# Performance work log

Measured on AMD Instinct MI355X. Metric: run time of the kernel, lower is better.

The kernel has to match this reference:

```python
import jax, jax.numpy as jnp
import numpy as np

B, F_IN, GRID, D, C = 32768, 64, 8, 16, 10
N = GRID * GRID          # 64 nodes
HID = N * D              # 1024
ATOMS = 2
LN_EPS = 1e-5
EPS = 1e-8


def _layernorm(h):
    mu = h.mean(-1, keepdims=True)
    var = h.var(-1, keepdims=True)
    return (h - mu) / jnp.sqrt(var + LN_EPS)


def _regulator(sig, w1, b1, g, be, w2, b2):
    # Linear -> LayerNorm -> Tanh -> Linear -> Sigmoid
    h = jnp.tanh(_layernorm(sig @ w1.T + b1) * g + be)
    return jax.nn.sigmoid(h @ w2.T + b2)


def _reg_params(key, in_dim):
    k = jax.random.split(key, 4)
    return (jax.random.normal(k[0], (16, in_dim)) * 0.3,
            jax.random.normal(k[1], (16,)) * 0.1,
            jnp.ones((16,)), jnp.zeros((16,)),
            jax.random.normal(k[2], (3, 16)) * 0.3,
            jax.random.normal(k[3], (3,)) * 0.1)


def setup_inputs() -> dict:
    key = jax.random.key(0)
    ks = jax.random.split(key, 16)
    # 2D grid 4-neighbour adjacency mask (constant)
    mask = np.zeros((N, N), np.float32)
    for i in range(N):
        r, c = divmod(i, GRID)
        if r > 0: mask[i, i - GRID] = 1
        if r < GRID - 1: mask[i, i + GRID] = 1
        if c > 0: mask[i, i - 1] = 1
        if c < GRID - 1: mask[i, i + 1] = 1
    pr = _reg_params(ks[10], 3)
    cr = _reg_params(ks[11], 3)
    sr = _reg_params(ks[12], 3)
    scr = _reg_params(ks[13], 2)
    inp = {
        "x": jax.random.normal(ks[0], (B, F_IN)),
        "W_embed": jax.random.normal(ks[1], (HID, F_IN)) * 0.1,
        "b_embed": jnp.zeros((HID,)),
        "adj_weights": jax.random.normal(ks[2], (N, N)) * 0.1,
        "adj_mask": jnp.asarray(mask),
        "V_slow": jax.random.normal(ks[3], (D, D)) * 0.1,
        "W_slow": jax.random.normal(ks[4], (D, D)) * 0.1,
        "gate_w": jax.random.normal(ks[5], (1, D)) * 0.3,
        "gate_b": jnp.zeros((1,)),
        "W_fast": jax.random.normal(ks[6], (D, D)) * 0.05,  # buffer, eval mode (no Hebbian update)
        "basis": jax.random.normal(ks[7], (ATOMS, D)) * 0.5,
        "Wq": jax.random.normal(ks[8], (D, D)) * 0.2,
        "sc_w1": jax.random.normal(ks[9], (8, HID)) * 0.05,
        "sc_w2": jax.random.normal(ks[14], (4, 8)) * 0.3,
        "W_read": jax.random.normal(ks[15], (C, HID)) * 0.05,
        "b_read": jnp.zeros((C,)),
    }
    for pre, p in (("pr", pr), ("cr", cr), ("sr", sr), ("scr", scr)):
        for nm, v in zip(("w1", "b1", "g", "be", "w2", "b2"), p):
            inp[pre + "_" + nm] = v
    return inp


def reference(x, W_embed, b_embed, adj_weights, adj_mask,
              pr_w1, pr_b1, pr_g, pr_be, pr_w2, pr_b2,
              V_slow, W_slow, gate_w, gate_b, W_fast,
              cr_w1, cr_b1, cr_g, cr_be, cr_w2, cr_b2,
              basis, Wq,
              sr_w1, sr_b1, sr_g, sr_be, sr_w2, sr_b2,
              sc_w1, sc_w2,
              scr_w1, scr_b1, scr_g, scr_be, scr_w2, scr_b2,
              W_read, b_read):
    Bx = x.shape[0]
    x_embed = (x @ W_embed.T + b_embed).reshape(Bx, N, D)

    # --- AutoregulatedPlasticity adjacency ---
    sig = jnp.stack([jnp.var(x, ddof=1), jnp.abs(x_embed).mean(),
                     jnp.linalg.norm(adj_weights)])[None]
    pl = _regulator(sig, pr_w1, pr_b1, pr_g, pr_be, pr_w2, pr_b2)[0]
    adj = jax.nn.sigmoid(adj_weights * pl[0]) * adj_mask
    adj = adj / jnp.clip(adj.sum(1, keepdims=True), 1e-6, None)
    x_agg = jnp.einsum('nm,bmd->bnd', adj, x_embed)

    # --- AutoregulatedContinuum (eval: W_fast fixed) ---
    xf = x_agg.reshape(-1, D)           # [B*N, D]
    v = xf @ V_slow.T
    sig = jnp.stack([jnp.var(xf, ddof=1), jnp.abs(v).mean(),
                     jnp.linalg.norm(W_slow)])[None]
    ctrl = _regulator(sig, cr_w1, cr_b1, cr_g, cr_be, cr_w2, cr_b2)[0]
    gate = jax.nn.sigmoid(v @ gate_w.T + gate_b) * ctrl[0]   # [B*N, 1]
    fast_out = xf @ W_fast.T
    x_proc = (gate * (v + fast_out * ctrl[2])).reshape(Bx, N, D)

    # --- AutoregulatedSymbiotic, applied per node (vmapped over node axis) ---
    ortho = jnp.linalg.norm(basis @ basis.T - jnp.eye(ATOMS))
    scale = D ** 0.5 + EPS

    def sym_one(xn):  # xn: [B, D]
        w = jax.nn.softmax((xn @ Wq.T) @ basis.T / scale, axis=-1)  # [B, ATOMS]
        ent = -(w * jnp.log(w + EPS)).sum(-1).mean()
        sig_n = jnp.stack([jnp.var(xn, ddof=1), ent, ortho])[None]
        infl = _regulator(sig_n, sr_w1, sr_b1, sr_g, sr_be, sr_w2, sr_b2)[0, 0]
        return (1.0 - infl) * xn + infl * (w @ basis), ent

    refined, ents = jax.vmap(sym_one)(x_proc.transpose(1, 0, 2))  # [N,B,D]
    x_proc = refined.transpose(1, 0, 2)
    entropy = ents[-1]  # torch loop keeps the last node's entropy

    x_flat = x_proc.reshape(Bx, HID)
    logits = x_flat @ W_read.T + b_read

    # --- AutoregulatedSupConHead (entropy.item() -> detached scalar) ---
    sigc = jnp.stack([jnp.var(x_flat, ddof=1),
                      jax.lax.stop_gradient(entropy)])[None]
    gain = _regulator(sigc, scr_w1, scr_b1, scr_g, scr_be, scr_w2, scr_b2)[0, 0]
    proj = (jax.nn.relu(x_flat @ sc_w1.T) @ sc_w2.T) * gain
    return logits, proj, entropy, ortho
```

## Files before the change

kernel.cpp:

```cpp
#include <hip/hip_runtime.h>

typedef unsigned short u16;
typedef unsigned long long u64;
typedef __attribute__((ext_vector_type(8))) short short8;
typedef __attribute__((ext_vector_type(4))) float f32x4;

#define MFMA16(a,b,c) __builtin_amdgcn_mfma_f32_16x16x32_bf16(a,b,c,0,0,0)

#define B_SZ   32768
#define NNODE  64
#define NB_PAIR (B_SZ*NNODE)
#define OUT_PROJ   327680
#define OUT_ENT    458752
#define OUT_ORTHO  458753

#define OFF_SCAL   ((size_t)0)
#define OFF_ADJ    ((size_t)512)
#define OFF_BEFF   (OFF_ADJ  + 8192u)
#define OFF_WEFF   (OFF_BEFF + 4096u)
#define OFF_WCAT   (OFF_WEFF + 131072u)
#define OFF_S1     (OFF_WCAT + 65536u)
#define OFF_S2     (OFF_S1   + 12288u)
#define OFF_S3     (OFF_S2   + 12288u)
#define OFF_S4     (OFF_S3   + 2048u*192u*4u)
#define OFF_H      (OFF_S4   + 8192u)
#define OFF_W01    (OFF_H    + (size_t)B_SZ*8u*4u)
#define OFF_CAN    (OFF_W01  + (size_t)NB_PAIR*4u)

#define CAN_X      0u
#define CAN_WEMB   2097152u
#define CAN_WREAD  (CAN_WEMB + 65536u)
#define CAN_SCW1   (CAN_WREAD + 10240u)
#define CAN_SMALL  (CAN_SCW1 + 8192u)
#define CAN_TOTAL  (CAN_SMALL + 11008u)
#define OFF_BEX    (((OFF_CAN + (size_t)CAN_TOTAL*2u) + 63u) & ~(size_t)63u)
#define OFF_WET    (OFF_BEX + 48u*16u*2u)
#define OFF_VW     (OFF_WET + 131072u)
#define OFF_VB     (OFF_VW  + 131072u)
#define OFF_WC     (OFF_VB  + 4096u)
#define OFF_SW     (OFF_WC  + 131072u)
#define OFF_BC2    (OFF_SW  + 24576u)
#define OFF_SB     (OFF_BC2 + 4096u)
#define OFF_DR     (OFF_SB  + 1024u)
#define WS_NEEDED  (OFF_DR  + 192u*8u)

__device__ __forceinline__ float bf2f(u16 u){
    unsigned v = ((unsigned)u) << 16;
    return __builtin_bit_cast(float, v);
}
__device__ __forceinline__ u16 f2bf(float f){
    unsigned u = __builtin_bit_cast(unsigned, f);
    u += 0x7FFFu + ((u >> 16) & 1u);
    return (u16)(u >> 16);
}
__device__ __forceinline__ float sigm(float x){ return 1.f/(1.f + expf(-x)); }
__device__ __forceinline__ u16 conv_one(const void* src, int i, int isfp32){
    return isfp32 ? f2bf(((const float*)src)[i]) : ((const u16*)src)[i];
}
__device__ __forceinline__ void store_out(void* dout, int idx, float v, int isfp32){
    if (isfp32) ((float*)dout)[idx] = v;
    else        ((u16*)dout)[idx]   = f2bf(v);
}
__device__ __forceinline__ double blk_red(double v, double* sred, int tid){
    #pragma unroll
    for (int off = 32; off > 0; off >>= 1) v += __shfl_xor(v, off);
    if ((tid & 63) == 0) sred[tid >> 6] = v;
    __syncthreads();
    double r = sred[0] + sred[1] + sred[2] + sred[3];
    __syncthreads();
    return r;
}
__device__ __forceinline__ void blk_red4(double* v, double* sred, int tid){
    #pragma unroll
    for (int off = 32; off > 0; off >>= 1){
        v[0] += __shfl_xor(v[0], off);
        v[1] += __shfl_xor(v[1], off);
        v[2] += __shfl_xor(v[2], off);
        v[3] += __shfl_xor(v[3], off);
    }
    if ((tid & 63) == 0){
        int w = tid >> 6;
        sred[w*4+0] = v[0]; sred[w*4+1] = v[1];
        sred[w*4+2] = v[2]; sred[w*4+3] = v[3];
    }
    __syncthreads();
    #pragma unroll
    for (int k = 0; k < 4; ++k)
        v[k] = sred[0*4+k] + sred[1*4+k] + sred[2*4+k] + sred[3*4+k];
    __syncthreads();
}

__device__ void run_regulator(const u16* w1, const u16* b1, const u16* g,
                              const u16* be, const u16* w2, const u16* b2,
                              const float* sig, int in_dim, float* out)
{
    float h[16];
    float mu = 0.f;
    for (int i = 0; i < 16; ++i){
        float a = bf2f(b1[i]);
        for (int j = 0; j < in_dim; ++j) a += sig[j]*bf2f(w1[i*in_dim + j]);
        h[i] = a; mu += a;
    }
    mu *= 0.0625f;
    float var = 0.f;
    for (int i = 0; i < 16; ++i){ float d = h[i]-mu; var += d*d; }
    var *= 0.0625f;
    float inv = 1.f / sqrtf(var + 1e-5f);
    for (int i = 0; i < 16; ++i){
        float hn = (h[i]-mu)*inv;
        h[i] = tanhf(hn*bf2f(g[i]) + bf2f(be[i]));
    }
    for (int c = 0; c < 3; ++c){
        float o = bf2f(b2[c]);
        for (int i = 0; i < 16; ++i) o += h[i]*bf2f(w2[c*16 + i]);
        out[c] = sigm(o);
    }
}

__device__ __forceinline__ int probe_isfp32(const u16* xraw, int tid, int* sred)
{
    int c = 0;
    #pragma unroll
    for (int j = 0; j < 4; ++j){
        u16 u = xraw[(tid*4 + j)*2];
        int e = (u >> 7) & 0xFF;
        if (u == 0 || (e >= 90 && e <= 140)) c++;
    }
    #pragma unroll
    for (int off = 32; off > 0; off >>= 1) c += __shfl_xor(c, off);
    if ((tid & 63) == 0) sred[tid >> 6] = c;
    __syncthreads();
    int tot = sred[0]+sred[1]+sred[2]+sred[3];
    __syncthreads();
    return tot < 614;
}

struct SmallTab { const void* src[36]; int cnt[36]; int off[36]; };
__global__ __launch_bounds__(256) void kc_all(SmallTab t,
    const void* x, const void* wemb, const void* wread_raw, const void* scw1_raw,
    const void* vslow_raw, const void* gatew_raw,
    u16* can, float* scal, u16* wcat, u16* wembT, u16* bex)
{
    __shared__ int sred[4];
    int b = blockIdx.x, tid = threadIdx.x;
    int isfp32 = probe_isfp32((const u16*)x, tid, sred);
    if (b == 0 && tid == 0) scal[127] = isfp32 ? 1.0f : 0.0f;
    if (b < 1024){
        int gid = b*256 + tid, stride = 1024*256;
        for (int i = gid; i < 2097152; i += stride) can[CAN_X + i]     = conv_one(x, i, isfp32);
        for (int i = gid; i < 65536;   i += stride) can[CAN_WEMB + i]  = conv_one(wemb, i, isfp32);
        for (int i = gid; i < 10240;   i += stride) can[CAN_WREAD + i] = conv_one(wread_raw, i, isfp32);
        for (int i = gid; i < 8192;    i += stride) can[CAN_SCW1 + i]  = conv_one(scw1_raw, i, isfp32);
    } else if (b < 1040){
        int gid = (b-1024)*256 + tid, stride = 16*256;
        for (int e = 0; e < 36; ++e){
            const void* s = t.src[e];
            u16* d = can + t.off[e];
            int n = t.cnt[e];
            for (int i = gid; i < n; i += stride) d[i] = conv_one(s, i, isfp32);
        }
    } else if (b < 1168){
        int idx = (b-1040)*256 + tid;
        int row = idx >> 10, k = idx & 1023;
        u16 v = 0;
        if (row < 10)      v = conv_one(wread_raw, row*1024 + k, isfp32);
        else if (row < 18) v = conv_one(scw1_raw, (row-10)*1024 + k, isfp32);
        int lo = k & 31;
        int khw = ((lo >> 2) & 3)*8 + ((lo >> 4) << 2) + (lo & 3);
        wcat[row*1024 + (k & ~31) + khw] = v;
    } else if (b < 1424){
        int idx = (b-1168)*256 + tid;
        int m = idx >> 10, jj = idx & 1023;
        wembT[jj*64 + m] = conv_one(wemb, m*1024 + jj, isfp32);
    } else {
        if (tid < 16){
            float a = 0.f;
            for (int i = 0; i < 16; ++i)
                a += bf2f(conv_one(gatew_raw, i, isfp32))*bf2f(conv_one(vslow_raw, i*16+tid, isfp32));
            bex[32*16+tid] = f2bf(a);
        }
    }
}

__global__ __launch_bounds__(256) void k1_embed(const u16* x, const u16* wemb,
                                                const u16* bemb, float* s1)
{
    __shared__ float red[12];
    int tid = threadIdx.x, wave = tid>>6, lane = tid&63;
    int m = lane&15, quad = lane>>4;
    int cg = blockIdx.x & 15, rc = blockIdx.x >> 4;
    short8 b0[4], b1[4];
    float bias[4];
    #pragma unroll
    for (int s = 0; s < 4; ++s){
        int col = cg*64 + s*16 + m;
        b0[s] = *(const short8*)(wemb + col*64 + quad*8);
        b1[s] = *(const short8*)(wemb + col*64 + quad*8 + 32);
        bias[s] = bf2f(bemb[col]);
    }
    float sx = 0.f, sxx = 0.f, sabs = 0.f;
    const u16* xbase = x + (size_t)(rc*512 + wave*128 + m)*64 + quad*8;
    #pragma unroll 4
    for (int it = 0; it < 8; ++it){
        const u16* xr = xbase + (size_t)it*16*64;
        short8 a0 = *(const short8*)xr;
        short8 a1 = *(const short8*)(xr + 32);
        if (cg == 0){
            #pragma unroll
            for (int j = 0; j < 8; ++j){
                float f0 = bf2f((u16)a0[j]); sx += f0; sxx += f0*f0;
                float f1 = bf2f((u16)a1[j]); sx += f1; sxx += f1*f1;
            }
        }
        #pragma unroll
        for (int s = 0; s < 4; ++s){
            f32x4 zc = {0.f,0.f,0.f,0.f};
            f32x4 c = MFMA16(a0, b0[s], zc);
            c = MFMA16(a1, b1[s], c);
            #pragma unroll
            for (int r = 0; r < 4; ++r)
                sabs += fabsf(c[r]+bias[s]);
        }
    }
    #pragma unroll
    for (int off = 32; off > 0; off >>= 1){
        sx   += __shfl_xor(sx, off);
        sxx  += __shfl_xor(sxx, off);
        sabs += __shfl_xor(sabs, off);
    }
    if (lane == 0){ red[wave*3] = sx; red[wave*3+1] = sxx; red[wave*3+2] = sabs; }
    __syncthreads();
    if (tid == 0){
        for (int k = 0; k < 3; ++k)
            s1[blockIdx.x*3 + k] = red[k] + red[3+k] + red[6+k] + red[9+k];
    }
}

__global__ __launch_bounds__(256) void k2_adj(const u16* adjw, const u16* adjm, const u16* bemb,
    const u16* w1, const u16* b1, const u16* g, const u16* be, const u16* w2, const u16* b2,
    const float* s1, float* scal, u16* adjb, float* beff)
{
    __shared__ double sred[16];
    __shared__ float raw[4096];
    __shared__ float rowsum[64];
    __shared__ float bembs[1024];
    __shared__ float pl0s;
    int tid = threadIdx.x;
    for (int i = tid; i < 1024; i += 256) bembs[i] = bf2f(bemb[i]);
    double v[4] = {0,0,0,0};
    for (int i = tid; i < 1024; i += 256){
        v[0] += (double)s1[i*3]; v[1] += (double)s1[i*3+1]; v[2] += (double)s1[i*3+2];
    }
    for (int i = tid; i < 4096; i += 256){ float f = bf2f(adjw[i]); v[3] += (double)(f*f); }
    blk_red4(v, sred, tid);
    if (tid == 0){
        double nx = 2097152.0;
        float sg[3];
        sg[0] = (float)((v[1] - v[0]*v[0]/nx)/(nx - 1.0));
        sg[1] = (float)(v[2] / 33554432.0);
        sg[2] = sqrtf((float)v[3]);
        float o[3];
        run_regulator(w1,b1,g,be,w2,b2, sg, 3, o);
        scal[0] = o[0]; pl0s = o[0];
    }
    __syncthreads();
    float pl0 = pl0s;
    for (int i = tid; i < 4096; i += 256)
        raw[i] = sigm(bf2f(adjw[i])*pl0) * bf2f(adjm[i]);
    __syncthreads();
    if (tid < 64){
        float r = 0.f;
        for (int mc = 0; mc < 64; ++mc) r += raw[tid*64 + mc];
        rowsum[tid] = fmaxf(r, 1e-6f);
    }
    __syncthreads();
    for (int i = tid; i < 4096; i += 256) adjb[i] = f2bf(raw[i] / rowsum[i>>6]);
    for (int o = tid; o < 1024; o += 256){
        int n = o >> 4, d = o & 15;
        float a = 0.f;
        for (int m = 0; m < 64; ++m) a += raw[n*64+m]*bembs[m*16+d];
        beff[o] = a / rowsum[n];
    }
}

__global__ __launch_bounds__(256) void k2b_mfma(const u16* adjb, const u16* wembT, u16* weff)
{
    int tid = threadIdx.x, wave = tid>>6, lane = tid&63;
    int m = lane&15, quad = lane>>4;
    const u16* ar = adjb + (wave*16 + m)*64 + quad*8;
    short8 a0 = *(const short8*)ar;
    short8 a1 = *(const short8*)(ar + 32);
    int col = blockIdx.x*16 + m;
    const u16* br = wembT + col*64 + quad*8;
    short8 b0 = *(const short8*)br;
    short8 b1 = *(const short8*)(br + 32);
    f32x4 acc = {0.f,0.f,0.f,0.f};
    acc = MFMA16(a0, b0, acc);
    acc = MFMA16(a1, b1, acc);
    #pragma unroll
    for (int r = 0; r < 4; ++r)
        weff[(size_t)(wave*16 + quad*4 + r)*1024 + blockIdx.x*16 + m] = f2bf(acc[r]);
}

__global__ __launch_bounds__(256) void kvw(const u16* vslow, const u16* weff, const float* beff,
                                           u16* vw, float* vbias)
{
    __shared__ float Vs[256];
    int tid = threadIdx.x, b = blockIdx.x;
    Vs[tid] = bf2f(vslow[tid]);
    __syncthreads();
    if (b < 256){
        int idx = b*256 + tid;
        int j = idx >> 6, kf = idx & 63;
        int n = j >> 4, i = j & 15;
        float a = 0.f;
        #pragma unroll
        for (int d = 0; d < 16; ++d) a += Vs[i*16+d]*bf2f(weff[(size_t)(n*16+d)*64 + kf]);
        vw[(size_t)j*64 + kf] = f2bf(a);
    } else {
        int o = (b-256)*256 + tid;
        int n = o >> 4, i = o & 15;
        float a = 0.f;
        #pragma unroll
        for (int d = 0; d < 16; ++d) a += Vs[i*16+d]*beff[n*16+d];
        vbias[o] = a;
    }
}

__global__ __launch_bounds__(256) void k3_stats(const u16* x, const u16* weff, const float* beff,
                                                const u16* vw, const float* vbias, float* s2)
{
    __shared__ float red[12];
    int tid = threadIdx.x, wave = tid>>6, lane = tid&63;
    int m = lane&15, quad = lane>>4;
    int cg = blockIdx.x & 15, rc = blockIdx.x >> 4;
    short8 wb0[4], wb1[4], vb0[4], vb1[4];
    float bev[4], vbv[4];
    #pragma unroll
    for (int s = 0; s < 4; ++s){
        int col = cg*64 + s*16 + m;
        wb0[s] = *(const short8*)(weff + (size_t)col*64 + quad*8);
        wb1[s] = *(const short8*)(weff + (size_t)col*64 + quad*8 + 32);
        vb0[s] = *(const short8*)(vw + (size_t)col*64 + quad*8);
        vb1[s] = *(const short8*)(vw + (size_t)col*64 + quad*8 + 32);
        bev[s] = beff[col];
        vbv[s] = vbias[col];
    }
    float psum=0.f, pssq=0.f, pabsv=0.f;
    const u16* xbase = x + (size_t)(rc*512 + wave*128 + m)*64 + quad*8;
    #pragma unroll 4
    for (int it = 0; it < 8; ++it){
        const u16* xr = xbase + (size_t)it*16*64;
        short8 a0 = *(const short8*)xr;
        short8 a1 = *(const short8*)(xr + 32);
        #pragma unroll
        for (int s = 0; s < 4; ++s){
            f32x4 zc = {0.f,0.f,0.f,0.f};
            f32x4 c = MFMA16(a0, wb0[s], zc);
            c = MFMA16(a1, wb1[s], c);
            f32x4 w = MFMA16(a0, vb0[s], zc);
            w = MFMA16(a1, vb1[s], w);
            #pragma unroll
            for (int r = 0; r < 4; ++r){
                float f0 = c[r] + bev[s];
                psum += f0; pssq += f0*f0;
                pabsv += fabsf(w[r] + vbv[s]);
            }
        }
    }
    #pragma unroll
    for (int off = 32; off > 0; off >>= 1){
        psum  += __shfl_xor(psum, off);
        pssq  += __shfl_xor(pssq, off);
        pabsv += __shfl_xor(pabsv, off);
    }
    if (lane == 0){ red[wave*3] = psum; red[wave*3+1] = pssq; red[wave*3+2] = pabsv; }
    __syncthreads();
    if (tid == 0){
        for (int k = 0; k < 3; ++k)
            s2[blockIdx.x*3 + k] = red[k] + red[3+k] + red[6+k] + red[9+k];
    }
}

__global__ __launch_bounds__(256) void k3b_ctrl(const u16* wslow,
    const u16* vslow, const u16* wfast, const u16* wq, const u16* basis,
    const u16* w1, const u16* b1, const u16* g, const u16* be, const u16* w2, const u16* b2,
    const float* s2, float* scal, u16* bex)
{
    __shared__ double sred[16];
    __shared__ float ctrl2s;
    int tid = threadIdx.x;
    double v[4] = {0,0,0,0};
    for (int i = tid; i < 1024; i += 256){
        v[0] += (double)s2[i*3]; v[1] += (double)s2[i*3+1]; v[2] += (double)s2[i*3+2];
    }
    float wf = bf2f(wslow[tid]);
    v[3] = (double)(wf*wf);
    blk_red4(v, sred, tid);
    if (tid == 0){
        double M = 33554432.0;
        float sg[3];
        sg[0] = (float)((v[1] - v[0]*v[0]/M)/(M - 1.0));
        sg[1] = (float)(v[2] / M);
        sg[2] = sqrtf((float)v[3]);
        float o[3];
        run_regulator(w1,b1,g,be,w2,b2, sg, 3, o);
        scal[1] = o[0]; scal[2] = o[2];
        ctrl2s = o[2];
    }
    __syncthreads();
    float ctrl2 = ctrl2s;
    if (tid < 64){
        #pragma unroll
        for (int j = 0; j < 4; ++j){
            int idx = tid*4 + j;
            int d = idx >> 4, k = idx & 15;
            bex[(16+d)*16+k] = f2bf(bf2f(vslow[idx]) + ctrl2*bf2f(wfast[idx]));
        }
    } else if (tid < 96){
        int a = (tid-64) >> 4, k = (tid-64) & 15;
        float e = 0.f;
        for (int d = 0; d < 16; ++d){
            float bq = 0.f;
            for (int j = 0; j < 16; ++j) bq += bf2f(basis[a*16+j])*bf2f(wq[j*16+d]);
            e += bq*(bf2f(vslow[d*16+k]) + ctrl2*bf2f(wfast[d*16+k]));
        }
        bex[(33+a)*16+k] = f2bf(0.25f*e);
    }
}

__global__ __launch_bounds__(256) void kbw(const u16* bex, const u16* weff, const float* beff,
                                           const u16* gateb, u16* wc, u16* sw,
                                           float* bc, float* sb)
{
    __shared__ float BcL[256], gvL[16], e0L[16], e1L[16];
    int tid = threadIdx.x;
    if (tid < 256) BcL[tid] = bf2f(bex[(16 + (tid>>4))*16 + (tid&15)]);
    if (tid < 16){
        gvL[tid] = bf2f(bex[32*16+tid]);
        e0L[tid] = bf2f(bex[33*16+tid]);
        e1L[tid] = bf2f(bex[34*16+tid]);
    }
    __syncthreads();
    int id = blockIdx.x*256 + tid;
    if (id < 65536){
        int col = id >> 6, k = id & 63;
        int n = col >> 4, d = col & 15;
        float a = 0.f;
        #pragma unroll
        for (int dd = 0; dd < 16; ++dd)
            a += BcL[d*16+dd]*bf2f(weff[(size_t)(n*16+dd)*64 + k]);
        wc[(size_t)col*64 + k] = f2bf(a);
    } else if (id < 77824){
        int j2 = id - 65536;
        int scol = j2 >> 6, k = j2 & 63;
        int n = scol/3, j = scol - n*3;
        const float* sr = (j==0) ? gvL : (j==1) ? e0L : e1L;
        float a = 0.f;
        #pragma unroll
        for (int dd = 0; dd < 16; ++dd)
            a += sr[dd]*bf2f(weff[(size_t)(n*16+dd)*64 + k]);
        sw[(size_t)scol*64 + k] = f2bf(a);
    } else if (id < 78848){
        int col = id - 77824;
        int n = col >> 4, d = col & 15;
        float a = 0.f;
        #pragma unroll
        for (int dd = 0; dd < 16; ++dd) a += BcL[d*16+dd]*beff[n*16+dd];
        bc[col] = a;
    } else if (id < 79040){
        int s = id - 78848;
        int n = s/3, j = s - n*3;
        const float* sr = (j==0) ? gvL : (j==1) ? e0L : e1L;
        float a = 0.f;
        #pragma unroll
        for (int dd = 0; dd < 16; ++dd) a += sr[dd]*beff[n*16+dd];
        if (j == 0) a += bf2f(gateb[0]);
        sb[s] = a;
    }
}

#define SCP 193
#define GTP 65
__global__ __launch_bounds__(256) void k4_stats(const u16* x, const u16* wc, const u16* sw,
    const float* bc, const float* sb, const float* scal, unsigned* wpack, float* s3)
{
    __shared__ float sc[32*SCP];
    __shared__ float gt[32*GTP];
    __shared__ float entp[256];
    __shared__ float snode[128];
    int tid = threadIdx.x, wave = tid>>6, lane = tid&63;
    int m = lane&15, quad = lane>>4;
    int row0 = blockIdx.x*32;
    const u16* xrA = x + (size_t)(row0 + m)*64 + quad*8;
    short8 a0A = *(const short8*)xrA;
    short8 a1A = *(const short8*)(xrA + 32);
    const u16* xrB = xrA + 16*64;
    short8 a0B = *(const short8*)xrB;
    short8 a1B = *(const short8*)(xrB + 32);
    float ctrl0 = scal[1];
    #pragma unroll
    for (int tt = 0; tt < 3; ++tt){
        int ct = wave*3 + tt;
        int scol = ct*16 + m;
        const u16* br = sw + (size_t)scol*64 + quad*8;
        short8 b0 = *(const short8*)br;
        short8 b1 = *(const short8*)(br + 32);
        f32x4 zc = {0.f,0.f,0.f,0.f};
        f32x4 cA = MFMA16(a0A, b0, zc);
        cA = MFMA16(a1A, b1, cA);
        f32x4 cB = MFMA16(a0B, b0, zc);
        cB = MFMA16(a1B, b1, cB);
        float sbv = sb[scol];
        #pragma unroll
        for (int r = 0; r < 4; ++r){
            sc[(quad*4+r)*SCP + scol]      = cA[r] + sbv;
            sc[(16+quad*4+r)*SCP + scol]   = cB[r] + sbv;
        }
    }
    __syncthreads();
    {
        int n = tid & 63, rgrp = tid >> 6;
        float ent = 0.f;
        #pragma unroll
        for (int rr = 0; rr < 8; ++rr){
            int row = rgrp*8 + rr;
            float gd  = sc[row*SCP + 3*n];
            float e0d = sc[row*SCP + 3*n + 1];
            float e1d = sc[row*SCP + 3*n + 2];
            float gate = ctrl0 / (1.f + __expf(-gd));
            float l0 = gate*e0d, l1 = gate*e1d;
            float w1v = 1.f/(1.f + __expf(l0 - l1));
            float w0v = 1.f - w1v;
            ent += -(w0v*__logf(w0v + 1e-8f) + w1v*__logf(w1v + 1e-8f));
            gt[row*GTP + n] = gate;
            wpack[(size_t)(row0 + row)*64 + n] =
                ((unsigned)f2bf(w0v) << 16) | (unsigned)f2bf(gate);
        }
        entp[tid] = ent;
    }
    __syncthreads();
    #pragma unroll
    for (int tt = 0; tt < 16; ++tt){
        int n = wave*16 + tt;
        int col = n*16 + m;
        const u16* br = wc + (size_t)col*64 + quad*8;
        short8 b0 = *(const short8*)br;
        short8 b1 = *(const short8*)(br + 32);
        f32x4 zc = {0.f,0.f,0.f,0.f};
        f32x4 cA = MFMA16(a0A, b0, zc);
        cA = MFMA16(a1A, b1, cA);
        f32x4 cB = MFMA16(a0B, b0, zc);
        cB = MFMA16(a1B, b1, cB);
        float bcv = bc[col];
        float ps = 0.f, pq = 0.f;
        #pragma unroll
        for (int r = 0; r < 4; ++r){
            float gA  = gt[(quad*4+r)*GTP + n];
            float xpA = gA*(cA[r] + bcv);
            float gB  = gt[(16+quad*4+r)*GTP + n];
            float xpB = gB*(cB[r] + bcv);
            ps += xpA + xpB; pq += xpA*xpA + xpB*xpB;
        }
        #pragma unroll
        for (int off = 32; off > 0; off >>= 1){
            ps += __shfl_xor(ps, off);
            pq += __shfl_xor(pq, off);
        }
        if (lane == 0){ snode[n] = ps; snode[64+n] = pq; }
    }
    __syncthreads();
    if (tid < 192){
        float v;
        if (tid < 128) v = snode[tid];
        else { int n = tid-128; v = entp[n]+entp[64+n]+entp[128+n]+entp[192+n]; }
        s3[(size_t)blockIdx.x*192 + tid] = v;
    }
}

__global__ __launch_bounds__(256) void k5ab(const float* s3, const u16* basis,
    const u16* w1, const u16* b1, const u16* g, const u16* be, const u16* w2, const u16* b2,
    float* scal, void* dout)
{
    __shared__ double sred[12];
    int tid = threadIdx.x, n = blockIdx.x;
    int wave = tid >> 6, lane = tid & 63;
    double a0 = 0, a1 = 0, a2 = 0;
    for (int i = tid; i < 1024; i += 256){
        const float* r = s3 + (size_t)i*192;
        a0 += (double)r[n]; a1 += (double)r[64+n]; a2 += (double)r[128+n];
    }
    #pragma unroll
    for (int off = 32; off > 0; off >>= 1){
        a0 += __shfl_xor(a0, off);
        a1 += __shfl_xor(a1, off);
        a2 += __shfl_xor(a2, off);
    }
    if (lane == 0){ sred[wave*3] = a0; sred[wave*3+1] = a1; sred[wave*3+2] = a2; }
    __syncthreads();
    if (tid == 0){
        int isfp32 = scal[127] != 0.f;
        double sum = sred[0]+sred[3]+sred[6]+sred[9];
        double ssq = sred[1]+sred[4]+sred[7]+sred[10];
        double ent = sred[2]+sred[5]+sred[8]+sred[11];
        double Mn = 524288.0;
        float varn = (float)((ssq - sum*sum/Mn)/(Mn - 1.0));
        float entm = (float)(ent / 32768.0);
        float b0[16], b1v[16];
        for (int d = 0; d < 16; ++d){ b0[d] = bf2f(basis[d]); b1v[d] = bf2f(basis[16+d]); }
        float g00=0.f, g01=0.f, g11=0.f;
        for (int d = 0; d < 16; ++d){
            g00 += b0[d]*b0[d]; g01 += b0[d]*b1v[d]; g11 += b1v[d]*b1v[d];
        }
        float ortho = sqrtf((g00-1.f)*(g00-1.f) + 2.f*g01*g01 + (g11-1.f)*(g11-1.f));
        float sg[3] = {varn, entm, ortho};
        float o[3];
        run_regulator(w1,b1,g,be,w2,b2, sg, 3, o);
        scal[4+n] = o[0];
        if (n == 63){ scal[68] = entm;  store_out(dout, OUT_ENT,   entm,  isfp32); }
        if (n == 0) { scal[69] = ortho; store_out(dout, OUT_ORTHO, ortho, isfp32); }
    }
}

__global__ __launch_bounds__(128, 2) void k6_read(const u16* x, const unsigned* wpack,
    const u16* wc, const float* bc, const u16* wcatP,
    const u16* basis, const u16* bread, const float* scal,
    void* dout, float* hbuf, float* s4)
{
    __shared__ unsigned gwP[64*65];
    __shared__ float bc_s[1024];
    __shared__ float infl_s[64], b0s[16], b1s[16], brd[16];
    __shared__ float red[4];
    int tid = threadIdx.x;
    int isfp32 = scal[127] != 0.f;
    for (int i = tid; i < 4096; i += 128)
        gwP[(i >> 6)*65 + (i & 63)] = wpack[(size_t)blockIdx.x*4096 + i];
    for (int i = tid; i < 1024; i += 128) bc_s[i] = bc[i];
    if (tid < 64) infl_s[tid] = scal[4+tid];
    if (tid < 16){
        b0s[tid] = bf2f(basis[tid]);
        b1s[tid] = bf2f(basis[16+tid]);
        brd[tid] = (tid < 10) ? bf2f(bread[tid]) : 0.f;
    }
    __syncthreads();
    int wave = tid>>6, lane = tid&63;
    int m = lane&15, quad = lane>>4;
    int rowA = blockIdx.x*64 + wave*32 + m;
    const u16* xrA = x + (size_t)rowA*64 + quad*8;
    short8 a0A = *(const short8*)xrA;
    short8 a1A = *(const short8*)(xrA + 32);
    const u16* xrB = xrA + 16*64;
    short8 a0B = *(const short8*)xrB;
    short8 a1B = *(const short8*)(xrB + 32);
    float b0d[4], b1d[4];
    #pragma unroll
    for (int r = 0; r < 4; ++r){ b0d[r] = b0s[quad*4+r]; b1d[r] = b1s[quad*4+r]; }
    const unsigned* gwA = gwP + (wave*32 + m)*65;
    const unsigned* gwB = gwA + 16*65;
    f32x4 acc0A = {0.f,0.f,0.f,0.f}, acc1A = {0.f,0.f,0.f,0.f};
    f32x4 acc0B = {0.f,0.f,0.f,0.f}, acc1B = {0.f,0.f,0.f,0.f};
    float psum = 0.f, pssq = 0.f;
    for (int c8 = 0; c8 < 8; ++c8){
        unsigned pdaA[8], pdbA[8], pdaB[8], pdbB[8];
        #pragma unroll
        for (int hf = 0; hf < 2; ++hf){
            short8 wf0[4], wf1[4];
            f32x4 bc4[4];
            unsigned gvA[4], gvB[4];
            float fiv[4];
            #pragma unroll
            for (int j = 0; j < 4; ++j){
                int n = c8*8 + hf*4 + j;
                int col = n*16 + m;
                const u16* br = wc + (size_t)col*64 + quad*8;
                wf0[j] = *(const short8*)br;
                wf1[j] = *(const short8*)(br + 32);
                bc4[j] = *(const f32x4*)(bc_s + n*16 + quad*4);
                gvA[j] = gwA[n];
                gvB[j] = gwB[n];
                fiv[j] = infl_s[n];
            }
            f32x4 cA[4], cB[4];
            #pragma unroll
            for (int j = 0; j < 4; ++j){
                f32x4 zc = {0.f,0.f,0.f,0.f};
                cA[j] = MFMA16(wf0[j], a0A, zc);
                cB[j] = MFMA16(wf0[j], a0B, zc);
            }
            #pragma unroll
            for (int j = 0; j < 4; ++j){
                cA[j] = MFMA16(wf1[j], a1A, cA[j]);
                cB[j] = MFMA16(wf1[j], a1B, cB[j]);
            }
            #pragma unroll
            for (int j = 0; j < 4; ++j){
                int t = hf*4 + j;
                float fi = fiv[j];
                {
                    float gate = bf2f((u16)(gvA[j] & 0xFFFFu));
                    float w0v  = bf2f((u16)(gvA[j] >> 16));
                    float Am   = (1.f - fi)*gate;
                    float fw0 = fi*w0v;
                    float fw1 = fi - fw0;
                    float xf[4];
                    #pragma unroll
                    for (int r = 0; r < 4; ++r){
                        float base = fw0*b0d[r] + fw1*b1d[r];
                        float v = Am*(cA[j][r] + bc4[j][r]) + base;
                        psum += v; pssq += v*v;
                        xf[r] = v;
                    }
                    pdaA[t] = (unsigned)f2bf(xf[0]) | ((unsigned)f2bf(xf[1]) << 16);
                    pdbA[t] = (unsigned)f2bf(xf[2]) | ((unsigned)f2bf(xf[3]) << 16);
                }
                {
                    float gate = bf2f((u16)(gvB[j] & 0xFFFFu));
                    float w0v  = bf2f((u16)(gvB[j] >> 16));
                    float Am   = (1.f - fi)*gate;
                    float fw0 = fi*w0v;
                    float fw1 = fi - fw0;
                    float xf[4];
                    #pragma unroll
                    for (int r = 0; r < 4; ++r){
                        float base = fw0*b0d[r] + fw1*b1d[r];
                        float v = Am*(cB[j][r] + bc4[j][r]) + base;
                        psum += v; pssq += v*v;
                        xf[r] = v;
                    }
                    pdaB[t] = (unsigned)f2bf(xf[0]) | ((unsigned)f2bf(xf[1]) << 16);
                    pdbB[t] = (unsigned)f2bf(xf[2]) | ((unsigned)f2bf(xf[3]) << 16);
                }
            }
        }
        #pragma unroll
        for (int kk = 0; kk < 4; ++kk){
            int4 awA = make_int4((int)pdaA[2*kk], (int)pdbA[2*kk],
                                 (int)pdaA[2*kk+1], (int)pdbA[2*kk+1]);
            int4 awB = make_int4((int)pdaB[2*kk], (int)pdbB[2*kk],
                                 (int)pdaB[2*kk+1], (int)pdbB[2*kk+1]);
            short8 afA = __builtin_bit_cast(short8, awA);
            short8 afB = __builtin_bit_cast(short8, awB);
            const u16* wb = wcatP + m*1024 + c8*128 + kk*32 + quad*8;
            short8 bb0 = *(const short8*)wb;
            short8 bb1 = *(const short8*)(wb + 16*1024);
            acc0A = MFMA16(afA, bb0, acc0A);
            acc0B = MFMA16(afB, bb0, acc0B);
            acc1A = MFMA16(afA, bb1, acc1A);
            acc1B = MFMA16(afB, bb1, acc1B);
        }
    }
    int rowbaseA = blockIdx.x*64 + wave*32 + quad*4;
    #pragma unroll
    for (int r = 0; r < 4; ++r){
        int rowgA = rowbaseA + r;
        if (m < 10) store_out(dout, rowgA*10 + m, acc0A[r] + brd[m], isfp32);
        else        hbuf[rowgA*8 + (m-10)] = fmaxf(acc0A[r], 0.f);
        if (m < 2)  hbuf[rowgA*8 + 6 + m]  = fmaxf(acc1A[r], 0.f);
        int rowgB = rowgA + 16;
        if (m < 10) store_out(dout, rowgB*10 + m, acc0B[r] + brd[m], isfp32);
        else        hbuf[rowgB*8 + (m-10)] = fmaxf(acc0B[r], 0.f);
        if (m < 2)  hbuf[rowgB*8 + 6 + m]  = fmaxf(acc1B[r], 0.f);
    }
    #pragma unroll
    for (int off = 32; off > 0; off >>= 1){
        psum += __shfl_xor(psum, off);
        pssq += __shfl_xor(pssq, off);
    }
    if (lane == 0){ red[wave] = psum; red[2+wave] = pssq; }
    __syncthreads();
    if (tid == 0){
        s4[blockIdx.x*2]   = red[0]+red[1];
        s4[blockIdx.x*2+1] = red[2]+red[3];
    }
}

__global__ __launch_bounds__(256) void k8_proj(const float* hbuf, const u16* scw2,
    const u16* w1, const u16* b1, const u16* g, const u16* be, const u16* w2, const u16* b2,
    const float* s4, const float* scal, void* dout)
{
    __shared__ double sred[4];
    __shared__ float w2s[32];
    __shared__ float gains;
    int tid = threadIdx.x;
    int isfp32 = scal[127] != 0.f;
    if (tid < 32) w2s[tid] = bf2f(scw2[tid]);
    double s=0, ss=0;
    for (int i = tid; i < 512; i += 256){ s += (double)s4[i*2]; ss += (double)s4[i*2+1]; }
    double S  = blk_red(s,  sred, tid);
    double SS = blk_red(ss, sred, tid);
    if (tid == 0){
        double M = 33554432.0;
        float sg[2];
        sg[0] = (float)((SS - S*S/M)/(M - 1.0));
        sg[1] = scal[68];
        float o[3];
        run_regulator(w1,b1,g,be,w2,b2, sg, 2, o);
        gains = o[0];
    }
    __syncthreads();
    float gain = gains;
    int b = blockIdx.x*256 + tid;
    const float* h = hbuf + (size_t)b*8;
    float hv[8];
    #pragma unroll
    for (int k = 0; k < 8; ++k) hv[k] = h[k];
    #pragma unroll
    for (int i = 0; i < 4; ++i){
        float o = 0.f;
        #pragma unroll
        for (int k = 0; k < 8; ++k) o += hv[k]*w2s[i*8+k];
        store_out(dout, OUT_PROJ + b*4 + i, o*gain, isfp32);
    }
}

extern "C" void kernel_launch(void* const* d_in, const int* in_sizes, int n_in,
                              void* d_out, int out_size, void* d_ws, size_t ws_size,
                              hipStream_t stream)
{
    if (ws_size < WS_NEEDED) return;

    char* ws = (char*)d_ws;
    float* scal  = (float*)(ws + OFF_SCAL);
    u16*   adjb  = (u16*)  (ws + OFF_ADJ);
    float* beff  = (float*)(ws + OFF_BEFF);
    u16*   weff  = (u16*)  (ws + OFF_WEFF);
    u16*   wcat  = (u16*)  (ws + OFF_WCAT);
    float* s1    = (float*)(ws + OFF_S1);
    float* s2    = (float*)(ws + OFF_S2);
    float* s3    = (float*)(ws + OFF_S3);
    float* s4    = (float*)(ws + OFF_S4);
    float* hbuf  = (float*)(ws + OFF_H);
    unsigned* wpack = (unsigned*)(ws + OFF_W01);
    u16*   can   = (u16*)  (ws + OFF_CAN);
    u16*   bex   = (u16*)  (ws + OFF_BEX);
    u16*   wembT = (u16*)  (ws + OFF_WET);
    u16*   vw    = (u16*)  (ws + OFF_VW);
    float* vbias = (float*)(ws + OFF_VB);
    u16*   wc    = (u16*)  (ws + OFF_WC);
    u16*   sw    = (u16*)  (ws + OFF_SW);
    float* bc    = (float*)(ws + OFF_BC2);
    float* sb    = (float*)(ws + OFF_SB);

    static const int sidx[36] = {2,3,4,5,6,7,8,9,10,11,13,15,
        16,17,18,19,20,21, 22,23,24,25,26,27, 28,29,30,31,32,33, 34,35,36,37,38,39};
    static const int scnt[36] = {1024,4096,4096,256,256,16,1,256,32,256,32,10,
        48,16,16,16,48,3, 48,16,16,16,48,3, 48,16,16,16,48,3, 32,16,16,16,48,3};
    SmallTab t;
    const u16* canp[40];
    {
        int off = (int)CAN_SMALL;
        for (int j = 0; j < 36; ++j){
            t.src[j] = d_in[sidx[j]];
            t.cnt[j] = scnt[j];
            t.off[j] = off;
            canp[sidx[j]] = can + off;
            off += (scnt[j] + 7) & ~7;
        }
    }
    canp[0]  = can + CAN_X;
    canp[1]  = can + CAN_WEMB;
    canp[12] = can + CAN_SCW1;
    canp[14] = can + CAN_WREAD;

    const u16* pr_[6]; const u16* cr_[6]; const u16* sr_[6]; const u16* sc_[6];
    for (int i = 0; i < 6; ++i){
        pr_[i] = canp[16+i]; cr_[i] = canp[22+i];
        sr_[i] = canp[28+i]; sc_[i] = canp[34+i];
    }

    kc_all  <<<1425,256, 0, stream>>>(t, d_in[0], d_in[1], d_in[14], d_in[12],
                 d_in[5], d_in[7], can, scal, wcat, wembT, bex);
    k1_embed<<<1024,256, 0, stream>>>(canp[0], canp[1], canp[2], s1);
    k2_adj  <<<1,   256, 0, stream>>>(canp[3], canp[4], canp[2],
                 pr_[0],pr_[1],pr_[2],pr_[3],pr_[4],pr_[5], s1, scal, adjb, beff);
    k2b_mfma<<<64,  256, 0, stream>>>(adjb, wembT, weff);
    kvw     <<<260, 256, 0, stream>>>(canp[5], weff, beff, vw, vbias);
    k3_stats<<<1024,256, 0, stream>>>(canp[0], weff, beff, vw, vbias, s2);
    k3b_ctrl<<<1,   256, 0, stream>>>(canp[6], canp[5], canp[9], canp[11], canp[10],
                 cr_[0],cr_[1],cr_[2],cr_[3],cr_[4],cr_[5], s2, scal, bex);
    kbw     <<<312, 256, 0, stream>>>(bex, weff, beff, canp[8], wc, sw, bc, sb);
    k4_stats<<<1024,256, 0, stream>>>(canp[0], wc, sw, bc, sb, scal, wpack, s3);
    k5ab    <<<64,  256, 0, stream>>>(s3, canp[10],
                 sr_[0],sr_[1],sr_[2],sr_[3],sr_[4],sr_[5], scal, d_out);
    k6_read <<<512, 128, 0, stream>>>(canp[0], wpack, wc, bc, wcat, canp[10], canp[15],
                 scal, d_out, hbuf, s4);
    k8_proj <<<128, 256, 0, stream>>>(hbuf, canp[13],
                 sc_[0],sc_[1],sc_[2],sc_[3],sc_[4],sc_[5], s4, scal, d_out);
}
```

Before: 305.4 us.

## Double rows per wave in readout kernel and vectorize input conversion copies

The readout kernel now handles 128 rows per block (64 per wave, four 16-row tiles) instead of 64, so each loaded weight fragment is reused across four MFMA tiles. The grid is halved to 256 blocks and the final reduction loop is adjusted to match. Separately, the input conversion copies x and the large weights in 8-element vectors instead of one element at a time. The risks are higher register pressure from the extra accumulators and a grid of 256 blocks, which may underfill the GPU.

```diff
diff --git a/kernel.cpp b/kernel.cpp
--- a/kernel.cpp
+++ b/kernel.cpp
@@ -135,6 +135,26 @@
     return tot < 614;
 }
 
+__device__ __forceinline__ void copy_big(const void* src, u16* dst, int nvec,
+                                         int gid, int stride, int isfp32)
+{
+    if (!isfp32){
+        const short8* s = (const short8*)src;
+        for (int i = gid; i < nvec; i += stride) *(short8*)(dst + i*8) = s[i];
+    } else {
+        const f32x4* s = (const f32x4*)src;
+        for (int i = gid; i < nvec; i += stride){
+            f32x4 v0 = s[i*2], v1 = s[i*2+1];
+            u64 lo = (u64)f2bf(v0[0]) | ((u64)f2bf(v0[1])<<16) |
+                     ((u64)f2bf(v0[2])<<32) | ((u64)f2bf(v0[3])<<48);
+            u64 hi = (u64)f2bf(v1[0]) | ((u64)f2bf(v1[1])<<16) |
+                     ((u64)f2bf(v1[2])<<32) | ((u64)f2bf(v1[3])<<48);
+            *(u64*)(dst + i*8)     = lo;
+            *(u64*)(dst + i*8 + 4) = hi;
+        }
+    }
+}
+
 struct SmallTab { const void* src[36]; int cnt[36]; int off[36]; };
 __global__ __launch_bounds__(256) void kc_all(SmallTab t,
     const void* x, const void* wemb, const void* wread_raw, const void* scw1_raw,
@@ -147,10 +167,10 @@
     if (b == 0 && tid == 0) scal[127] = isfp32 ? 1.0f : 0.0f;
     if (b < 1024){
         int gid = b*256 + tid, stride = 1024*256;
-        for (int i = gid; i < 2097152; i += stride) can[CAN_X + i]     = conv_one(x, i, isfp32);
-        for (int i = gid; i < 65536;   i += stride) can[CAN_WEMB + i]  = conv_one(wemb, i, isfp32);
-        for (int i = gid; i < 10240;   i += stride) can[CAN_WREAD + i] = conv_one(wread_raw, i, isfp32);
-        for (int i = gid; i < 8192;    i += stride) can[CAN_SCW1 + i]  = conv_one(scw1_raw, i, isfp32);
+        copy_big(x,         can + CAN_X,     262144, gid, stride, isfp32);
+        copy_big(wemb,      can + CAN_WEMB,  8192,   gid, stride, isfp32);
+        copy_big(wread_raw, can + CAN_WREAD, 1280,   gid, stride, isfp32);
+        copy_big(scw1_raw,  can + CAN_SCW1,  1024,   gid, stride, isfp32);
     } else if (b < 1040){
         int gid = (b-1024)*256 + tid, stride = 16*256;
         for (int e = 0; e < 36; ++e){
@@ -622,19 +642,40 @@
     }
 }
 
+__device__ __forceinline__ void k6_epi(unsigned gv, float fi, f32x4 c, f32x4 bcv,
+    const float* b0d, const float* b1d, float& psum, float& pssq,
+    unsigned& lo, unsigned& hi)
+{
+    float gate = bf2f((u16)(gv & 0xFFFFu));
+    float w0v  = bf2f((u16)(gv >> 16));
+    float Am = (1.f - fi)*gate;
+    float fw0 = fi*w0v;
+    float fw1 = fi - fw0;
+    float xf[4];
+    #pragma unroll
+    for (int r = 0; r < 4; ++r){
+        float base = fw0*b0d[r] + fw1*b1d[r];
+        float v = Am*(c[r] + bcv[r]) + base;
+        psum += v; pssq += v*v;
+        xf[r] = v;
+    }
+    lo = (unsigned)f2bf(xf[0]) | ((unsigned)f2bf(xf[1]) << 16);
+    hi = (unsigned)f2bf(xf[2]) | ((unsigned)f2bf(xf[3]) << 16);
+}
+
 __global__ __launch_bounds__(128, 2) void k6_read(const u16* x, const unsigned* wpack,
     const u16* wc, const float* bc, const u16* wcatP,
     const u16* basis, const u16* bread, const float* scal,
     void* dout, float* hbuf, float* s4)
 {
-    __shared__ unsigned gwP[64*65];
+    __shared__ unsigned gwP[128*65];
     __shared__ float bc_s[1024];
     __shared__ float infl_s[64], b0s[16], b1s[16], brd[16];
     __shared__ float red[4];
     int tid = threadIdx.x;
     int isfp32 = scal[127] != 0.f;
-    for (int i = tid; i < 4096; i += 128)
-        gwP[(i >> 6)*65 + (i & 63)] = wpack[(size_t)blockIdx.x*4096 + i];
+    for (int i = tid; i < 8192; i += 128)
+        gwP[(i >> 6)*65 + (i & 63)] = wpack[(size_t)blockIdx.x*8192 + i];
     for (int i = tid; i < 1024; i += 128) bc_s[i] = bc[i];
     if (tid < 64) infl_s[tid] = scal[4+tid];
     if (tid < 16){
@@ -645,28 +686,31 @@
     __syncthreads();
     int wave = tid>>6, lane = tid&63;
     int m = lane&15, quad = lane>>4;
-    int rowA = blockIdx.x*64 + wave*32 + m;
+    int rowA = blockIdx.x*128 + wave*64 + m;
     const u16* xrA = x + (size_t)rowA*64 + quad*8;
-    short8 a0A = *(const short8*)xrA;
-    short8 a1A = *(const short8*)(xrA + 32);
-    const u16* xrB = xrA + 16*64;
-    short8 a0B = *(const short8*)xrB;
-    short8 a1B = *(const short8*)(xrB + 32);
+    short8 a0A = *(const short8*)xrA,            a1A = *(const short8*)(xrA + 32);
+    short8 a0B = *(const short8*)(xrA + 16*64),  a1B = *(const short8*)(xrA + 16*64 + 32);
+    short8 a0C = *(const short8*)(xrA + 32*64),  a1C = *(const short8*)(xrA + 32*64 + 32);
+    short8 a0D = *(const short8*)(xrA + 48*64),  a1D = *(const short8*)(xrA + 48*64 + 32);
     float b0d[4], b1d[4];
     #pragma unroll
     for (int r = 0; r < 4; ++r){ b0d[r] = b0s[quad*4+r]; b1d[r] = b1s[quad*4+r]; }
-    const unsigned* gwA = gwP + (wave*32 + m)*65;
+    const unsigned* gwA = gwP + (wave*64 + m)*65;
     const unsigned* gwB = gwA + 16*65;
-    f32x4 acc0A = {0.f,0.f,0.f,0.f}, acc1A = {0.f,0.f,0.f,0.f};
-    f32x4 acc0B = {0.f,0.f,0.f,0.f}, acc1B = {0.f,0.f,0.f,0.f};
+    const unsigned* gwC = gwA + 32*65;
+    const unsigned* gwD = gwA + 48*65;
+    f32x4 acc0A = {0,0,0,0}, acc1A = {0,0,0,0};
+    f32x4 acc0B = {0,0,0,0}, acc1B = {0,0,0,0};
+    f32x4 acc0C = {0,0,0,0}, acc1C = {0,0,0,0};
+    f32x4 acc0D = {0,0,0,0}, acc1D = {0,0,0,0};
     float psum = 0.f, pssq = 0.f;
     for (int c8 = 0; c8 < 8; ++c8){
         unsigned pdaA[8], pdbA[8], pdaB[8], pdbB[8];
+        unsigned pdaC[8], pdbC[8], pdaD[8], pdbD[8];
         #pragma unroll
         for (int hf = 0; hf < 2; ++hf){
             short8 wf0[4], wf1[4];
             f32x4 bc4[4];
-            unsigned gvA[4], gvB[4];
             float fiv[4];
             #pragma unroll
             for (int j = 0; j < 4; ++j){
@@ -676,90 +720,77 @@
                 wf0[j] = *(const short8*)br;
                 wf1[j] = *(const short8*)(br + 32);
                 bc4[j] = *(const f32x4*)(bc_s + n*16 + quad*4);
-                gvA[j] = gwA[n];
-                gvB[j] = gwB[n];
                 fiv[j] = infl_s[n];
             }
-            f32x4 cA[4], cB[4];
+            f32x4 cA[4], cB[4], cC[4], cD[4];
             #pragma unroll
             for (int j = 0; j < 4; ++j){
                 f32x4 zc = {0.f,0.f,0.f,0.f};
                 cA[j] = MFMA16(wf0[j], a0A, zc);
                 cB[j] = MFMA16(wf0[j], a0B, zc);
+                cC[j] = MFMA16(wf0[j], a0C, zc);
+                cD[j] = MFMA16(wf0[j], a0D, zc);
             }
             #pragma unroll
             for (int j = 0; j < 4; ++j){
                 cA[j] = MFMA16(wf1[j], a1A, cA[j]);
                 cB[j] = MFMA16(wf1[j], a1B, cB[j]);
+                cC[j] = MFMA16(wf1[j], a1C, cC[j]);
+                cD[j] = MFMA16(wf1[j], a1D, cD[j]);
             }
             #pragma unroll
             for (int j = 0; j < 4; ++j){
                 int t = hf*4 + j;
+                int n = c8*8 + t;
                 float fi = fiv[j];
-                {
-                    float gate = bf2f((u16)(gvA[j] & 0xFFFFu));
-                    float w0v  = bf2f((u16)(gvA[j] >> 16));
-                    float Am   = (1.f - fi)*gate;
-                    float fw0 = fi*w0v;
-                    float fw1 = fi - fw0;
-                    float xf[4];
-                    #pragma unroll
-                    for (int r = 0; r < 4; ++r){
-                        float base = fw0*b0d[r] + fw1*b1d[r];
-                        float v = Am*(cA[j][r] + bc4[j][r]) + base;
-                        psum += v; pssq += v*v;
-                        xf[r] = v;
-                    }
-                    pdaA[t] = (unsigned)f2bf(xf[0]) | ((unsigned)f2bf(xf[1]) << 16);
-                    pdbA[t] = (unsigned)f2bf(xf[2]) | ((unsigned)f2bf(xf[3]) << 16);
-                }
-                {
-                    float gate = bf2f((u16)(gvB[j] & 0xFFFFu));
-                    float w0v  = bf2f((u16)(gvB[j] >> 16));
-                    float Am   = (1.f - fi)*gate;
-                    float fw0 = fi*w0v;
-                    float fw1 = fi - fw0;
-                    float xf[4];
-                    #pragma unroll
-                    for (int r = 0; r < 4; ++r){
-                        float base = fw0*b0d[r] + fw1*b1d[r];
-                        float v = Am*(cB[j][r] + bc4[j][r]) + base;
-                        psum += v; pssq += v*v;
-                        xf[r] = v;
-                    }
-                    pdaB[t] = (unsigned)f2bf(xf[0]) | ((unsigned)f2bf(xf[1]) << 16);
-                    pdbB[t] = (unsigned)f2bf(xf[2]) | ((unsigned)f2bf(xf[3]) << 16);
-                }
+                k6_epi(gwA[n], fi, cA[j], bc4[j], b0d, b1d, psum, pssq, pdaA[t], pdbA[t]);
+                k6_epi(gwB[n], fi, cB[j], bc4[j], b0d, b1d, psum, pssq, pdaB[t], pdbB[t]);
+                k6_epi(gwC[n], fi, cC[j], bc4[j], b0d, b1d, psum, pssq, pdaC[t], pdbC[t]);
+                k6_epi(gwD[n], fi, cD[j], bc4[j], b0d, b1d, psum, pssq, pdaD[t], pdbD[t]);
             }
         }
         #pragma unroll
         for (int kk = 0; kk < 4; ++kk){
-            int4 awA = make_int4((int)pdaA[2*kk], (int)pdbA[2*kk],
-                                 (int)pdaA[2*kk+1], (int)pdbA[2*kk+1]);
-            int4 awB = make_int4((int)pdaB[2*kk], (int)pdbB[2*kk],
-                                 (int)pdaB[2*kk+1], (int)pdbB[2*kk+1]);
-            short8 afA = __builtin_bit_cast(short8, awA);
-            short8 afB = __builtin_bit_cast(short8, awB);
+            short8 afA = __builtin_bit_cast(short8, make_int4((int)pdaA[2*kk], (int)pdbA[2*kk],
+                                 (int)pdaA[2*kk+1], (int)pdbA[2*kk+1]));
+            short8 afB = __builtin_bit_cast(short8, make_int4((int)pdaB[2*kk], (int)pdbB[2*kk],
+                                 (int)pdaB[2*kk+1], (int)pdbB[2*kk+1]));
+            short8 afC = __builtin_bit_cast(short8, make_int4((int)pdaC[2*kk], (int)pdbC[2*kk],
+                                 (int)pdaC[2*kk+1], (int)pdbC[2*kk+1]));
+            short8 afD = __builtin_bit_cast(short8, make_int4((int)pdaD[2*kk], (int)pdbD[2*kk],
+                                 (int)pdaD[2*kk+1], (int)pdbD[2*kk+1]));
             const u16* wb = wcatP + m*1024 + c8*128 + kk*32 + quad*8;
             short8 bb0 = *(const short8*)wb;
             short8 bb1 = *(const short8*)(wb + 16*1024);
             acc0A = MFMA16(afA, bb0, acc0A);
             acc0B = MFMA16(afB, bb0, acc0B);
+            acc0C = MFMA16(afC, bb0, acc0C);
+            acc0D = MFMA16(afD, bb0, acc0D);
             acc1A = MFMA16(afA, bb1, acc1A);
             acc1B = MFMA16(afB, bb1, acc1B);
-        }
-    }
-    int rowbaseA = blockIdx.x*64 + wave*32 + quad*4;
+            acc1C = MFMA16(afC, bb1, acc1C);
+            acc1D = MFMA16(afD, bb1, acc1D);
+        }
+    }
+    int rowbase = blockIdx.x*128 + wave*64 + quad*4;
     #pragma unroll
     for (int r = 0; r < 4; ++r){
-        int rowgA = rowbaseA + r;
-        if (m < 10) store_out(dout, rowgA*10 + m, acc0A[r] + brd[m], isfp32);
-        else        hbuf[rowgA*8 + (m-10)] = fmaxf(acc0A[r], 0.f);
-        if (m < 2)  hbuf[rowgA*8 + 6 + m]  = fmaxf(acc1A[r], 0.f);
-        int rowgB = rowgA + 16;
-        if (m < 10) store_out(dout, rowgB*10 + m, acc0B[r] + brd[m], isfp32);
-        else        hbuf[rowgB*8 + (m-10)] = fmaxf(acc0B[r], 0.f);
-        if (m < 2)  hbuf[rowgB*8 + 6 + m]  = fmaxf(acc1B[r], 0.f);
+        int rowg = rowbase + r;
+        if (m < 10) store_out(dout, rowg*10 + m, acc0A[r] + brd[m], isfp32);
+        else        hbuf[rowg*8 + (m-10)] = fmaxf(acc0A[r], 0.f);
+        if (m < 2)  hbuf[rowg*8 + 6 + m]  = fmaxf(acc1A[r], 0.f);
+        rowg += 16;
+        if (m < 10) store_out(dout, rowg*10 + m, acc0B[r] + brd[m], isfp32);
+        else        hbuf[rowg*8 + (m-10)] = fmaxf(acc0B[r], 0.f);
+        if (m < 2)  hbuf[rowg*8 + 6 + m]  = fmaxf(acc1B[r], 0.f);
+        rowg += 16;
+        if (m < 10) store_out(dout, rowg*10 + m, acc0C[r] + brd[m], isfp32);
+        else        hbuf[rowg*8 + (m-10)] = fmaxf(acc0C[r], 0.f);
+        if (m < 2)  hbuf[rowg*8 + 6 + m]  = fmaxf(acc1C[r], 0.f);
+        rowg += 16;
+        if (m < 10) store_out(dout, rowg*10 + m, acc0D[r] + brd[m], isfp32);
+        else        hbuf[rowg*8 + (m-10)] = fmaxf(acc0D[r], 0.f);
+        if (m < 2)  hbuf[rowg*8 + 6 + m]  = fmaxf(acc1D[r], 0.f);
     }
     #pragma unroll
     for (int off = 32; off > 0; off >>= 1){
@@ -785,7 +816,7 @@
     int isfp32 = scal[127] != 0.f;
     if (tid < 32) w2s[tid] = bf2f(scw2[tid]);
     double s=0, ss=0;
-    for (int i = tid; i < 512; i += 256){ s += (double)s4[i*2]; ss += (double)s4[i*2+1]; }
+    for (int i = tid; i < 256; i += 256){ s += (double)s4[i*2]; ss += (double)s4[i*2+1]; }
     double S  = blk_red(s,  sred, tid);
     double SS = blk_red(ss, sred, tid);
     if (tid == 0){
@@ -882,7 +913,7 @@
     k4_stats<<<1024,256, 0, stream>>>(canp[0], wc, sw, bc, sb, scal, wpack, s3);
     k5ab    <<<64,  256, 0, stream>>>(s3, canp[10],
                  sr_[0],sr_[1],sr_[2],sr_[3],sr_[4],sr_[5], scal, d_out);
-    k6_read <<<512, 128, 0, stream>>>(canp[0], wpack, wc, bc, wcat, canp[10], canp[15],
+    k6_read <<<256, 128, 0, stream>>>(canp[0], wpack, wc, bc, wcat, canp[10], canp[15],
                  scal, d_out, hbuf, s4);
     k8_proj <<<128, 256, 0, stream>>>(hbuf, canp[13],
                  sc_[0],sc_[1],sc_[2],sc_[3],sc_[4],sc_[5], s4, scal, d_out);
```

Measured after the change: 329.3 us. 7.8% more time.
